# Performance work log

Measured on AMD Instinct MI355X. Metric: run time of the kernel, lower is better.

The kernel has to match this reference:

```python
import jax, jax.numpy as jnp
import numpy as np


def _conv(x, w, stride=1, pad=0):
    return jax.lax.conv_general_dilated(
        x, w, window_strides=(stride, stride),
        padding=[(pad, pad), (pad, pad)],
        dimension_numbers=('NCHW', 'OIHW', 'NCHW'))


def _frozen_bn(x, gamma, beta, mean, var):
    # FrozenBatchNorm2d: scale = gamma * rsqrt(var); bias = beta - mean*scale
    scale = gamma * jax.lax.rsqrt(var)
    bias = beta - mean * scale
    return x * scale[None, :, None, None] + bias[None, :, None, None]


def setup_inputs() -> dict:
    key = jax.random.key(0)
    ks = jax.random.split(key, 16)
    N, Cin, H, W = 32, 1024, 28, 28
    Cb, Cout = 256, 1024
    x = jax.random.normal(ks[0], (N, Cin, H, W), dtype=jnp.float32)
    # conv weights, kaiming-uniform-ish scale
    w1 = jax.random.uniform(ks[1], (Cb, Cin, 1, 1), minval=-1, maxval=1) * (1.0 / np.sqrt(Cin))
    w2 = jax.random.uniform(ks[2], (Cb, Cb, 3, 3), minval=-1, maxval=1) * (1.0 / np.sqrt(Cb * 9))
    w3 = jax.random.uniform(ks[3], (Cout, Cb, 1, 1), minval=-1, maxval=1) * (1.0 / np.sqrt(Cb))
    def bn_params(k, n):
        k1, k2, k3, k4 = jax.random.split(k, 4)
        gamma = jax.random.uniform(k1, (n,), minval=0.5, maxval=1.5)
        beta = jax.random.normal(k2, (n,)) * 0.1
        mean = jax.random.normal(k3, (n,)) * 0.1
        var = jax.random.uniform(k4, (n,), minval=0.5, maxval=1.5)
        return gamma, beta, mean, var
    g1, b1, m1, v1 = bn_params(ks[4], Cb)
    g2, b2, m2, v2 = bn_params(ks[5], Cb)
    g3, b3, m3, v3 = bn_params(ks[6], Cout)
    return dict(x=x, w1=w1, w2=w2, w3=w3,
                g1=g1, b1=b1, m1=m1, v1=v1,
                g2=g2, b2=b2, m2=m2, v2=v2,
                g3=g3, b3=b3, m3=m3, v3=v3)


def reference(x, w1, w2, w3, g1, b1, m1, v1, g2, b2, m2, v2, g3, b3, m3, v3):
    identity = x
    out = _conv(x, w1, stride=1, pad=0)          # 1x1: Cin -> Cb
    out = jax.nn.relu(_frozen_bn(out, g1, b1, m1, v1))
    out = _conv(out, w2, stride=1, pad=1)        # 3x3: Cb -> Cb
    out = jax.nn.relu(_frozen_bn(out, g2, b2, m2, v2))
    out = _conv(out, w3, stride=1, pad=0)        # 1x1: Cb -> Cout
    out = _frozen_bn(out, g3, b3, m3, v3)
    # stride==1 and in_channels==out_channels -> downsample is None
    out = jax.nn.relu(out + identity)
    return out
```

## Files before the change

kernel.cpp:

```cpp
#include <hip/hip_runtime.h>


#define BM 128
#define BNT 128
#define BK 64

typedef __attribute__((ext_vector_type(8))) short short8;
typedef __attribute__((ext_vector_type(4))) float f32x4;

__device__ inline unsigned short f2bf(float f) {
    unsigned int u = __float_as_uint(f);
    u += 0x7fff + ((u >> 16) & 1);
    return (unsigned short)(u >> 16);
}

__device__ inline void gload16(const unsigned short* g, unsigned short* l) {
    __builtin_amdgcn_global_load_lds(
        (const __attribute__((address_space(1))) unsigned int*)g,
        (__attribute__((address_space(3))) unsigned int*)l, 16, 0, 0);
}

__global__ __launch_bounds__(256) void prep_x(const float* __restrict__ x,
                                              unsigned short* __restrict__ Xh) {
    __shared__ float t[32][33];
    const int p0 = blockIdx.x * 32, c0 = blockIdx.y * 32, n = blockIdx.z;
    const int tid = threadIdx.x;
    const int pl = tid & 31, cl = tid >> 5;
    const float* xb = x + ((size_t)n * 1024 + c0) * 784;
    #pragma unroll
    for (int j = 0; j < 4; ++j) {
        int ci = cl + j * 8;
        int p = p0 + pl;
        t[ci][pl] = (p < 784) ? xb[(size_t)ci * 784 + p] : 0.f;
    }
    __syncthreads();
    const int cl2 = tid & 31, pl2 = tid >> 5;
    #pragma unroll
    for (int j = 0; j < 4; ++j) {
        int p = p0 + pl2 + j * 8;
        if (p < 784)
            Xh[(size_t)(n * 784 + p) * 1024 + c0 + cl2] = f2bf(t[cl2][pl2 + j * 8]);
    }
}

__global__ __launch_bounds__(256) void prep_w(
    const float* __restrict__ w1, const float* __restrict__ w2, const float* __restrict__ w3,
    const float* g1, const float* b1, const float* m1, const float* v1,
    const float* g2, const float* b2, const float* m2, const float* v2,
    const float* g3, const float* b3, const float* m3, const float* v3,
    unsigned short* __restrict__ Wb1, unsigned short* __restrict__ Wt2,
    unsigned short* __restrict__ Wb3,
    float* __restrict__ bn1, float* __restrict__ bn2, float* __restrict__ bn3) {
    int i = blockIdx.x * 256 + threadIdx.x;
    if (i < 262144) Wb1[i] = f2bf(w1[i]);
    if (i < 589824) {
        int kw = i % 3, t1 = i / 3;
        int kh = t1 % 3, t2 = t1 / 3;
        int ci = t2 & 255, co = t2 >> 8;
        Wt2[(size_t)((kh * 3 + kw) * 256 + co) * 256 + ci] = f2bf(w2[i]);
    }
    if (i < 262144) Wb3[i] = f2bf(w3[i]);
    if (i < 256) { float s = g1[i] * rsqrtf(v1[i]); bn1[i] = s; bn1[256 + i] = b1[i] - m1[i] * s; }
    if (i < 256) { float s = g2[i] * rsqrtf(v2[i]); bn2[i] = s; bn2[256 + i] = b2[i] - m2[i] * s; }
    if (i < 1024) { float s = g3[i] * rsqrtf(v3[i]); bn3[i] = s; bn3[1024 + i] = b3[i] - m3[i] * s; }
}

__global__ __launch_bounds__(256) void zero16(uint4* __restrict__ p, int n) {
    int i = blockIdx.x * 256 + threadIdx.x;
    if (i < n) p[i] = make_uint4(0u, 0u, 0u, 0u);
}

template <int CX, int NTAPS, int LAYER>
__global__ __launch_bounds__(256) void conv_mfma(
    const unsigned short* __restrict__ Xg, const unsigned short* __restrict__ Wg,
    const float* __restrict__ bn, int nco,
    const float* __restrict__ residual,
    unsigned short* __restrict__ obf, float* __restrict__ ofp) {
    __shared__ __align__(16) unsigned short Xs[BM * BK];
    __shared__ __align__(16) unsigned short Ws[BNT * BK];
    const int tid = threadIdx.x;
    const int wave = tid >> 6, lane = tid & 63;
    const int quad = lane >> 4, l15 = lane & 15;
    const int Pb = blockIdx.x * BM;
    const int cb = blockIdx.y * BNT;
    const int wco = (wave & 1) * 64;
    const int wpx = (wave >> 1) * 64;

    int rowt[4], cso[4];
    size_t xrow[4];
    #pragma unroll
    for (int t = 0; t < 4; ++t) {
        int slot = t * 256 + tid;
        int row = slot >> 3;
        int c = slot & 7;
        rowt[t] = row;
        cso[t] = ((c ^ (row & 7)) * 8);
        if (LAYER == 2) {
            int P = Pb + row;
            int n = P / 784, rem = P - n * 784;
            int h = rem / 28, w = rem - h * 28;
            xrow[t] = (size_t)n * 900 + h * 30 + w;
        } else {
            xrow[t] = (size_t)(Pb + row);
        }
    }

    f32x4 acc[4][4];
    #pragma unroll
    for (int i = 0; i < 4; ++i)
        #pragma unroll
        for (int j = 0; j < 4; ++j)
            acc[i][j] = (f32x4){0.f, 0.f, 0.f, 0.f};

    for (int tap = 0; tap < NTAPS; ++tap) {
        const int tapofs = (NTAPS == 9) ? ((tap / 3) * 30 + (tap % 3)) : 0;
        const unsigned short* Wtap = Wg + (size_t)tap * 256 * CX;
        for (int k0 = 0; k0 < CX; k0 += BK) {
            __syncthreads();
            #pragma unroll
            for (int t = 0; t < 4; ++t) {
                unsigned short* xl = Xs + (size_t)(t * 256 + wave * 64) * 8;
                unsigned short* wl = Ws + (size_t)(t * 256 + wave * 64) * 8;
                const unsigned short* gx = Xg + (xrow[t] + tapofs) * (size_t)CX + k0 + cso[t];
                const unsigned short* gw = Wtap + (size_t)(cb + rowt[t]) * CX + k0 + cso[t];
                gload16(gx, xl);
                gload16(gw, wl);
            }
            __syncthreads();
            #pragma unroll
            for (int kk = 0; kk < BK; kk += 32) {
                short8 af[4], bf[4];
                const int cbase = kk >> 3;
                #pragma unroll
                for (int wi = 0; wi < 4; ++wi) {
                    int row = wco + wi * 16 + l15;
                    int ch = (cbase + quad) ^ (row & 7);
                    af[wi] = *(const short8*)(Ws + (row * 8 + ch) * 8);
                }
                #pragma unroll
                for (int wj = 0; wj < 4; ++wj) {
                    int row = wpx + wj * 16 + l15;
                    int ch = (cbase + quad) ^ (row & 7);
                    bf[wj] = *(const short8*)(Xs + (row * 8 + ch) * 8);
                }
                #pragma unroll
                for (int wi = 0; wi < 4; ++wi)
                    #pragma unroll
                    for (int wj = 0; wj < 4; ++wj)
                        acc[wi][wj] = __builtin_amdgcn_mfma_f32_16x16x32_bf16(
                            af[wi], bf[wj], acc[wi][wj], 0, 0, 0);
            }
        }
    }

    #pragma unroll
    for (int wi = 0; wi < 4; ++wi) {
        int co0 = cb + wco + wi * 16 + quad * 4;
        f32x4 sc = *(const f32x4*)(bn + co0);
        f32x4 bi = *(const f32x4*)(bn + nco + co0);
        #pragma unroll
        for (int wj = 0; wj < 4; ++wj) {
            int P = Pb + wpx + wj * 16 + l15;
            if (LAYER == 3) {
                int n = P / 784, p = P - n * 784;
                #pragma unroll
                for (int r = 0; r < 4; ++r) {
                    size_t off = ((size_t)n * 1024 + co0 + r) * 784 + p;
                    float v = fmaf(acc[wi][wj][r], sc[r], bi[r]) + residual[off];
                    ofp[off] = v > 0.f ? v : 0.f;
                }
            } else {
                size_t orow;
                if (LAYER == 1) {
                    int n = P / 784, rem = P - n * 784;
                    int h = rem / 28, w = rem - h * 28;
                    orow = (size_t)n * 900 + (h + 1) * 30 + (w + 1);
                } else {
                    orow = (size_t)P;
                }
                float v0 = fmaf(acc[wi][wj][0], sc[0], bi[0]); v0 = v0 > 0.f ? v0 : 0.f;
                float v1 = fmaf(acc[wi][wj][1], sc[1], bi[1]); v1 = v1 > 0.f ? v1 : 0.f;
                float v2 = fmaf(acc[wi][wj][2], sc[2], bi[2]); v2 = v2 > 0.f ? v2 : 0.f;
                float v3 = fmaf(acc[wi][wj][3], sc[3], bi[3]); v3 = v3 > 0.f ? v3 : 0.f;
                uint2 pk;
                pk.x = (unsigned)f2bf(v0) | ((unsigned)f2bf(v1) << 16);
                pk.y = (unsigned)f2bf(v2) | ((unsigned)f2bf(v3) << 16);
                *(uint2*)(obf + orow * 256 + co0) = pk;
            }
        }
    }
}

extern "C" void kernel_launch(void* const* d_in, const int* in_sizes, int n_in,
                              void* d_out, int out_size, void* d_ws, size_t ws_size,
                              hipStream_t stream) {
    const float* x  = (const float*)d_in[0];
    const float* w1 = (const float*)d_in[1];
    const float* w2 = (const float*)d_in[2];
    const float* w3 = (const float*)d_in[3];
    const float* g1 = (const float*)d_in[4];  const float* b1 = (const float*)d_in[5];
    const float* m1 = (const float*)d_in[6];  const float* v1 = (const float*)d_in[7];
    const float* g2 = (const float*)d_in[8];  const float* b2 = (const float*)d_in[9];
    const float* m2 = (const float*)d_in[10]; const float* v2 = (const float*)d_in[11];
    const float* g3 = (const float*)d_in[12]; const float* b3 = (const float*)d_in[13];
    const float* m3 = (const float*)d_in[14]; const float* v3 = (const float*)d_in[15];
    float* out = (float*)d_out;

    char* ws = (char*)d_ws;
    unsigned short* Xh  = (unsigned short*)(ws);
    unsigned short* y1p = (unsigned short*)(ws + 51380224);
    unsigned short* y2  = (unsigned short*)(ws + 66125824);
    unsigned short* Wb1 = (unsigned short*)(ws + 78970880);
    unsigned short* Wt2 = (unsigned short*)(ws + 79495168);
    unsigned short* Wb3 = (unsigned short*)(ws + 80674816);
    float* bn1 = (float*)(ws + 81199104);
    float* bn2 = (float*)(ws + 81201152);
    float* bn3 = (float*)(ws + 81203200);

    prep_x<<<dim3(25, 32, 32), 256, 0, stream>>>(x, Xh);
    prep_w<<<2304, 256, 0, stream>>>(w1, w2, w3,
                                     g1, b1, m1, v1, g2, b2, m2, v2, g3, b3, m3, v3,
                                     Wb1, Wt2, Wb3, bn1, bn2, bn3);
    zero16<<<3600, 256, 0, stream>>>((uint4*)y1p, 921600);

    conv_mfma<1024, 1, 1><<<dim3(196, 2), 256, 0, stream>>>(
        Xh, Wb1, bn1, 256, nullptr, y1p, nullptr);
    conv_mfma<256, 9, 2><<<dim3(196, 2), 256, 0, stream>>>(
        y1p, Wt2, bn2, 256, nullptr, y2, nullptr);
    conv_mfma<256, 1, 3><<<dim3(196, 8), 256, 0, stream>>>(
        y2, Wb3, bn3, 1024, x, nullptr, out);
}
```

Before: 355.1 us.

## Stage conv epilogues through LDS for coalesced vector stores and packed prep stores

The conv epilogues now write BN-scaled results into shared memory in two passes, then read them back so each thread issues 16-byte coalesced global stores. For layer 3 this also lets the residual read and fp32 output write use float4 accesses instead of strided scalar ones. prep_x packs two bf16 values per 32-bit store. The cost is extra LDS traffic, more barriers and slightly more shared memory for layer 3, which may reduce occupancy.

```diff
diff --git a/kernel.cpp b/kernel.cpp
--- a/kernel.cpp
+++ b/kernel.cpp
@@ -34,12 +34,15 @@
         t[ci][pl] = (p < 784) ? xb[(size_t)ci * 784 + p] : 0.f;
     }
     __syncthreads();
-    const int cl2 = tid & 31, pl2 = tid >> 5;
+    const int c2 = (tid & 15) * 2, pr = tid >> 4;
     #pragma unroll
-    for (int j = 0; j < 4; ++j) {
-        int p = p0 + pl2 + j * 8;
-        if (p < 784)
-            Xh[(size_t)(n * 784 + p) * 1024 + c0 + cl2] = f2bf(t[cl2][pl2 + j * 8]);
+    for (int j = 0; j < 2; ++j) {
+        int p = p0 + pr + j * 16;
+        if (p < 784) {
+            unsigned int pk = (unsigned)f2bf(t[c2][pr + j * 16]) |
+                              ((unsigned)f2bf(t[c2 + 1][pr + j * 16]) << 16);
+            *(unsigned int*)(Xh + (size_t)(n * 784 + p) * 1024 + c0 + c2) = pk;
+        }
     }
 }
 
@@ -71,13 +74,14 @@
 }
 
 template <int CX, int NTAPS, int LAYER>
-__global__ __launch_bounds__(256) void conv_mfma(
+__device__ __forceinline__ void conv_body(
     const unsigned short* __restrict__ Xg, const unsigned short* __restrict__ Wg,
     const float* __restrict__ bn, int nco,
     const float* __restrict__ residual,
     unsigned short* __restrict__ obf, float* __restrict__ ofp) {
-    __shared__ __align__(16) unsigned short Xs[BM * BK];
-    __shared__ __align__(16) unsigned short Ws[BNT * BK];
+    __shared__ __align__(16) char smem[LAYER == 3 ? 33792 : 32768];
+    unsigned short* Xs = (unsigned short*)smem;
+    unsigned short* Ws = (unsigned short*)(smem + 16384);
     const int tid = threadIdx.x;
     const int wave = tid >> 6, lane = tid & 63;
     const int quad = lane >> 4, l15 = lane & 15;
@@ -153,23 +157,81 @@
         }
     }
 
-    #pragma unroll
-    for (int wi = 0; wi < 4; ++wi) {
-        int co0 = cb + wco + wi * 16 + quad * 4;
-        f32x4 sc = *(const f32x4*)(bn + co0);
-        f32x4 bi = *(const f32x4*)(bn + nco + co0);
+    __syncthreads();
+
+    if (LAYER == 3) {
+        float* ep = (float*)smem;
         #pragma unroll
-        for (int wj = 0; wj < 4; ++wj) {
-            int P = Pb + wpx + wj * 16 + l15;
-            if (LAYER == 3) {
-                int n = P / 784, p = P - n * 784;
-                #pragma unroll
-                for (int r = 0; r < 4; ++r) {
-                    size_t off = ((size_t)n * 1024 + co0 + r) * 784 + p;
-                    float v = fmaf(acc[wi][wj][r], sc[r], bi[r]) + residual[off];
-                    ofp[off] = v > 0.f ? v : 0.f;
-                }
-            } else {
+        for (int pass = 0; pass < 2; ++pass) {
+            if ((wave & 1) == pass) {
+                #pragma unroll
+                for (int wi = 0; wi < 4; ++wi) {
+                    int co0 = cb + wco + wi * 16 + quad * 4;
+                    f32x4 sc = *(const f32x4*)(bn + co0);
+                    f32x4 bi = *(const f32x4*)(bn + nco + co0);
+                    int cr0 = wi * 16 + quad * 4;
+                    #pragma unroll
+                    for (int wj = 0; wj < 4; ++wj) {
+                        int px = wpx + wj * 16 + l15;
+                        #pragma unroll
+                        for (int r = 0; r < 4; ++r)
+                            ep[(cr0 + r) * 132 + px] = fmaf(acc[wi][wj][r], sc[r], bi[r]);
+                    }
+                }
+            }
+            __syncthreads();
+            {
+                int cr = tid >> 2;
+                int cg = tid & 3;
+                int co = cb + pass * 64 + cr;
+                #pragma unroll
+                for (int k = 0; k < 8; ++k) {
+                    int px4 = (cg + 4 * k) * 4;
+                    f32x4 v = *(const f32x4*)(ep + cr * 132 + px4);
+                    int P = Pb + px4;
+                    int n = P / 784, p = P - n * 784;
+                    size_t off = ((size_t)n * 1024 + co) * 784 + p;
+                    float4 rs = *(const float4*)(residual + off);
+                    float4 o;
+                    o.x = v[0] + rs.x; o.x = o.x > 0.f ? o.x : 0.f;
+                    o.y = v[1] + rs.y; o.y = o.y > 0.f ? o.y : 0.f;
+                    o.z = v[2] + rs.z; o.z = o.z > 0.f ? o.z : 0.f;
+                    o.w = v[3] + rs.w; o.w = o.w > 0.f ? o.w : 0.f;
+                    *(float4*)(ofp + off) = o;
+                }
+            }
+            __syncthreads();
+        }
+    } else {
+        unsigned short* ep = (unsigned short*)smem;
+        #pragma unroll
+        for (int pass = 0; pass < 2; ++pass) {
+            if ((wave >> 1) == pass) {
+                #pragma unroll
+                for (int wi = 0; wi < 4; ++wi) {
+                    int co0 = cb + wco + wi * 16 + quad * 4;
+                    f32x4 sc = *(const f32x4*)(bn + co0);
+                    f32x4 bi = *(const f32x4*)(bn + nco + co0);
+                    int col = wco + wi * 16 + quad * 4;
+                    #pragma unroll
+                    for (int wj = 0; wj < 4; ++wj) {
+                        int pxl = wj * 16 + l15;
+                        float v0 = fmaf(acc[wi][wj][0], sc[0], bi[0]); v0 = v0 > 0.f ? v0 : 0.f;
+                        float v1 = fmaf(acc[wi][wj][1], sc[1], bi[1]); v1 = v1 > 0.f ? v1 : 0.f;
+                        float v2 = fmaf(acc[wi][wj][2], sc[2], bi[2]); v2 = v2 > 0.f ? v2 : 0.f;
+                        float v3 = fmaf(acc[wi][wj][3], sc[3], bi[3]); v3 = v3 > 0.f ? v3 : 0.f;
+                        uint2 pk;
+                        pk.x = (unsigned)f2bf(v0) | ((unsigned)f2bf(v1) << 16);
+                        pk.y = (unsigned)f2bf(v2) | ((unsigned)f2bf(v3) << 16);
+                        *(uint2*)(ep + pxl * 136 + col) = pk;
+                    }
+                }
+            }
+            __syncthreads();
+            {
+                int pxl = tid >> 2;
+                int cg = tid & 3;
+                int P = Pb + pass * 64 + pxl;
                 size_t orow;
                 if (LAYER == 1) {
                     int n = P / 784, rem = P - n * 784;
@@ -178,17 +240,33 @@
                 } else {
                     orow = (size_t)P;
                 }
-                float v0 = fmaf(acc[wi][wj][0], sc[0], bi[0]); v0 = v0 > 0.f ? v0 : 0.f;
-                float v1 = fmaf(acc[wi][wj][1], sc[1], bi[1]); v1 = v1 > 0.f ? v1 : 0.f;
-                float v2 = fmaf(acc[wi][wj][2], sc[2], bi[2]); v2 = v2 > 0.f ? v2 : 0.f;
-                float v3 = fmaf(acc[wi][wj][3], sc[3], bi[3]); v3 = v3 > 0.f ? v3 : 0.f;
-                uint2 pk;
-                pk.x = (unsigned)f2bf(v0) | ((unsigned)f2bf(v1) << 16);
-                pk.y = (unsigned)f2bf(v2) | ((unsigned)f2bf(v3) << 16);
-                *(uint2*)(obf + orow * 256 + co0) = pk;
-            }
-        }
-    }
+                #pragma unroll
+                for (int k = 0; k < 4; ++k) {
+                    int cc = (cg + 4 * k) * 8;
+                    uint4 v = *(const uint4*)(ep + pxl * 136 + cc);
+                    *(uint4*)(obf + orow * 256 + cb + cc) = v;
+                }
+            }
+            __syncthreads();
+        }
+    }
+}
+
+__global__ __launch_bounds__(256) void conv1_mfma(
+    const unsigned short* __restrict__ Xg, const unsigned short* __restrict__ Wg,
+    const float* __restrict__ bn, unsigned short* __restrict__ obf) {
+    conv_body<1024, 1, 1>(Xg, Wg, bn, 256, nullptr, obf, nullptr);
+}
+__global__ __launch_bounds__(256) void conv2_mfma(
+    const unsigned short* __restrict__ Xg, const unsigned short* __restrict__ Wg,
+    const float* __restrict__ bn, unsigned short* __restrict__ obf) {
+    conv_body<256, 9, 2>(Xg, Wg, bn, 256, nullptr, obf, nullptr);
+}
+__global__ __launch_bounds__(256) void conv3_mfma(
+    const unsigned short* __restrict__ Xg, const unsigned short* __restrict__ Wg,
+    const float* __restrict__ bn, const float* __restrict__ residual,
+    float* __restrict__ ofp) {
+    conv_body<256, 1, 3>(Xg, Wg, bn, 1024, residual, nullptr, ofp);
 }
 
 extern "C" void kernel_launch(void* const* d_in, const int* in_sizes, int n_in,
@@ -223,10 +301,7 @@
                                      Wb1, Wt2, Wb3, bn1, bn2, bn3);
     zero16<<<3600, 256, 0, stream>>>((uint4*)y1p, 921600);
 
-    conv_mfma<1024, 1, 1><<<dim3(196, 2), 256, 0, stream>>>(
-        Xh, Wb1, bn1, 256, nullptr, y1p, nullptr);
-    conv_mfma<256, 9, 2><<<dim3(196, 2), 256, 0, stream>>>(
-        y1p, Wt2, bn2, 256, nullptr, y2, nullptr);
-    conv_mfma<256, 1, 3><<<dim3(196, 8), 256, 0, stream>>>(
-        y2, Wb3, bn3, 1024, x, nullptr, out);
-}
+    conv1_mfma<<<dim3(196, 2), 256, 0, stream>>>(Xh, Wb1, bn1, y1p);
+    conv2_mfma<<<dim3(196, 2), 256, 0, stream>>>(y1p, Wt2, bn2, y2);
+    conv3_mfma<<<dim3(196, 8), 256, 0, stream>>>(y2, Wb3, bn3, x, out);
+}
```

New measurement: 343.2 us. -3.4%, faster.
